# Optimization experiments

Hardware: AMD Instinct MI355X
Metric: run time of the kernel (lower is better)

Reference implementation:

```python
import jax, jax.numpy as jnp
import numpy as np


def setup_inputs() -> dict:
    key = jax.random.key(0)
    k1, k2 = jax.random.split(key)
    B, N, D = 4, 2048, 1024
    context = jax.random.normal(k1, (B, N, D), dtype=jnp.float32)
    # Dense(embedding_dim*3): kernel [D, 3D], bias [3D] (glorot-ish scale)
    W_qkv = jax.random.normal(k2, (D, 3 * D), dtype=jnp.float32) * (1.0 / np.sqrt(D))
    b_qkv = jnp.zeros((3 * D,), dtype=jnp.float32)
    return {"context": context, "W_qkv": W_qkv, "b_qkv": b_qkv}


def reference(context, W_qkv, b_qkv):
    B, N, D = context.shape
    qkv = context @ W_qkv + b_qkv                       # [B, N, 3D]
    q, k, v = jnp.split(qkv, 3, axis=-1)                # each [B, N, D]
    scores = jnp.einsum("bnd,bmd->bnm", q, k)           # [B, N, N]
    # Faithful quirk: original divides by sqrt(scores.shape[-1]) == sqrt(N)
    scores = scores / jnp.asarray(np.sqrt(N), dtype=scores.dtype)
    causal = jnp.tril(jnp.ones((N, N), dtype=jnp.float32))  # lower-triangular
    scores = jnp.where(causal == 0, -jnp.inf, scores)
    probs = jax.nn.softmax(scores, axis=-1)             # [B, N, N]
    out = jnp.einsum("bnm,bmd->bnd", probs, v)          # [B, N, D]
    return out
```

## Files before the change

kernel.cpp:

```cpp
#include <hip/hip_runtime.h>
#include <cstdint>
#include <cstddef>


typedef __attribute__((ext_vector_type(8))) __bf16 bf16x8;
typedef __attribute__((ext_vector_type(4))) float f32x4;

__device__ inline unsigned short f2bf(float f) {
  unsigned u = __float_as_uint(f);
  u = (u + 0x7FFFu + ((u >> 16) & 1u)) >> 16;
  return (unsigned short)u;
}

__device__ inline void gld16(const void* g, void* l) {
  __builtin_amdgcn_global_load_lds(
      (const __attribute__((address_space(1))) unsigned int*)g,
      (__attribute__((address_space(3))) unsigned int*)l, 16, 0, 0);
}

__device__ inline void stage_tiles(unsigned short* As, unsigned short* Bs,
                                   const unsigned short* Abase, long strideA,
                                   const unsigned short* Bbase, long strideB,
                                   int k0, int wave, int lrow, int lcol) {
#pragma unroll
  for (int c = 0; c < 4; c++) {
    const int q = wave * 4 + c;
    const int row = q * 8 + lrow;
    gld16(Abase + (size_t)row * strideA + k0 + lcol, &As[q * 512]);
    gld16(Bbase + (size_t)row * strideB + k0 + lcol, &Bs[q * 512]);
  }
}

__device__ inline void compute_tiles(const unsigned short* As, const unsigned short* Bs,
                                     int lane, int ry, int rx, f32x4 acc[4][4]) {
#pragma unroll
  for (int kk = 0; kk < 64; kk += 32) {
    const int cbase = (kk >> 3) + (lane >> 4);
    const int csw = ((cbase ^ (lane & 7)) << 3);
    bf16x8 a[4], b[4];
#pragma unroll
    for (int mi = 0; mi < 4; mi++)
      a[mi] = *(const bf16x8*)&As[(ry + mi * 16 + (lane & 15)) * 64 + csw];
#pragma unroll
    for (int nj = 0; nj < 4; nj++)
      b[nj] = *(const bf16x8*)&Bs[(rx + nj * 16 + (lane & 15)) * 64 + csw];
#pragma unroll
    for (int mi = 0; mi < 4; mi++)
#pragma unroll
      for (int nj = 0; nj < 4; nj++)
        acc[mi][nj] = __builtin_amdgcn_mfma_f32_16x16x32_bf16(b[nj], a[mi], acc[mi][nj], 0, 0, 0);
  }
}

__device__ inline void mma_mainloop(unsigned short* As, unsigned short* Bs,
                                    const unsigned short* Abase, long strideA,
                                    const unsigned short* Bbase, long strideB,
                                    int kIters, f32x4 acc[4][4]) {
  const int lane = threadIdx.x & 63, wave = threadIdx.x >> 6;
  const int ry = (wave >> 1) * 64, rx = (wave & 1) * 64;
  const int lrow = lane >> 3;
  const int lcol = ((lane & 7) ^ lrow) * 8;
#pragma unroll
  for (int mi = 0; mi < 4; mi++)
#pragma unroll
    for (int nj = 0; nj < 4; nj++) acc[mi][nj] = (f32x4)(0.f);
  for (int kt = 0; kt < kIters; kt++) {
    __syncthreads();
    stage_tiles(As, Bs, Abase, strideA, Bbase, strideB, kt * 64, wave, lrow, lcol);
    __syncthreads();
    compute_tiles(As, Bs, lane, ry, rx, acc);
  }
}

__device__ inline void mma_mainloop_db(unsigned short* As0, unsigned short* Bs0,
                                       unsigned short* As1, unsigned short* Bs1,
                                       const unsigned short* Abase, long strideA,
                                       const unsigned short* Bbase, long strideB,
                                       int kIters, f32x4 acc[4][4]) {
  const int lane = threadIdx.x & 63, wave = threadIdx.x >> 6;
  const int ry = (wave >> 1) * 64, rx = (wave & 1) * 64;
  const int lrow = lane >> 3;
  const int lcol = ((lane & 7) ^ lrow) * 8;
#pragma unroll
  for (int mi = 0; mi < 4; mi++)
#pragma unroll
    for (int nj = 0; nj < 4; nj++) acc[mi][nj] = (f32x4)(0.f);
  stage_tiles(As0, Bs0, Abase, strideA, Bbase, strideB, 0, wave, lrow, lcol);
  for (int kt = 0; kt < kIters; kt++) {
    __syncthreads();
    unsigned short* Asc = (kt & 1) ? As1 : As0;
    unsigned short* Bsc = (kt & 1) ? Bs1 : Bs0;
    if (kt + 1 < kIters) {
      unsigned short* Asn = (kt & 1) ? As0 : As1;
      unsigned short* Bsn = (kt & 1) ? Bs0 : Bs1;
      stage_tiles(Asn, Bsn, Abase, strideA, Bbase, strideB, (kt + 1) * 64, wave, lrow, lcol);
    }
    compute_tiles(Asc, Bsc, lane, ry, rx, acc);
  }
}


__global__ void k_convert(const float* __restrict__ x, unsigned short* __restrict__ y, int n4) {
  int i = blockIdx.x * blockDim.x + threadIdx.x;
  if (i >= n4) return;
  float4 v = ((const float4*)x)[i];
  ushort4 o;
  o.x = f2bf(v.x); o.y = f2bf(v.y); o.z = f2bf(v.z); o.w = f2bf(v.w);
  ((ushort4*)y)[i] = o;
}

__global__ void k_transpose_w(const float* __restrict__ W, unsigned short* __restrict__ Wt) {
  __shared__ unsigned short sm[64 * 65];
  const int n0 = blockIdx.x * 64;
  const int k0 = blockIdx.y * 64;
  for (int i = threadIdx.x; i < 4096; i += 256) {
    int r = i >> 6, c = i & 63;
    sm[c * 65 + r] = f2bf(W[(size_t)(k0 + r) * 3072 + n0 + c]);
  }
  __syncthreads();
  for (int i = threadIdx.x; i < 4096; i += 256) {
    int r = i >> 6, c = i & 63;
    Wt[(size_t)(n0 + r) * 1024 + k0 + c] = sm[r * 65 + c];
  }
}


__global__ __launch_bounds__(256) void k_gemm_qkv(const unsigned short* __restrict__ A,
                                                  const unsigned short* __restrict__ Wt,
                                                  const float* __restrict__ bias,
                                                  unsigned short* __restrict__ qk,
                                                  unsigned short* __restrict__ vT) {
  __shared__ unsigned short As[128 * 64];
  __shared__ unsigned short Bs[128 * 64];
  f32x4 acc[4][4];
  const int tM0 = blockIdx.y * 128;
  const int lane = threadIdx.x & 63, wave = threadIdx.x >> 6;
  const int ry = (wave >> 1) * 64, rx = (wave & 1) * 64;
  const int l16 = lane & 15, rq = lane >> 4;
  const bool isQK = blockIdx.x < 16;
  const int tN0 = isQK ? blockIdx.x * 128 : (blockIdx.x - 16) * 128;
  const unsigned short* Wtile = Wt + (size_t)(isQK ? tN0 : 2048 + tN0) * 1024;

  mma_mainloop(As, Bs, A + (size_t)tM0 * 1024, 1024, Wtile, 1024, 16, acc);

  if (isQK) {
#pragma unroll
    for (int mi = 0; mi < 4; mi++) {
      const int m = tM0 + ry + mi * 16 + l16;
#pragma unroll
      for (int nj = 0; nj < 4; nj++) {
        const int n = tN0 + rx + nj * 16 + rq * 4;
        const float4 bv = *(const float4*)&bias[n];
        ushort4 o;
        o.x = f2bf(acc[mi][nj][0] + bv.x);
        o.y = f2bf(acc[mi][nj][1] + bv.y);
        o.z = f2bf(acc[mi][nj][2] + bv.z);
        o.w = f2bf(acc[mi][nj][3] + bv.w);
        *(ushort4*)&qk[(size_t)m * 2048 + n] = o;
      }
    }
  } else {
#pragma unroll
    for (int mi = 0; mi < 4; mi++) {
      const int m = tM0 + ry + mi * 16 + l16;
      const int b = m >> 11, ns = m & 2047;
#pragma unroll
      for (int nj = 0; nj < 4; nj++) {
        const int d0 = tN0 + rx + nj * 16 + rq * 4;
        const float4 bv = *(const float4*)&bias[2048 + d0];
#pragma unroll
        for (int r = 0; r < 4; r++)
          vT[((size_t)(b * 1024 + d0 + r)) * 2048 + ns] = f2bf(acc[mi][nj][r] + ((const float*)&bv)[r]);
      }
    }
  }
}

__global__ __launch_bounds__(256) void k_scores(const unsigned short* __restrict__ qk,
                                                unsigned short* __restrict__ P,
                                                float* __restrict__ l, float scale) {
  __shared__ unsigned short As0[128 * 64], Bs0[128 * 64];
  __shared__ unsigned short As1[128 * 64], Bs1[128 * 64];
  const int t = blockIdx.x, b = blockIdx.z;
  int qb = (int)((sqrtf(8.0f * (float)t + 1.0f) - 1.0f) * 0.5f);
  while (qb * (qb + 1) / 2 > t) qb--;
  while ((qb + 1) * (qb + 2) / 2 <= t) qb++;
  const int kb = t - qb * (qb + 1) / 2;
  f32x4 acc[4][4];
  const unsigned short* Aq = qk + ((size_t)(b * 2048 + qb * 128)) * 2048;
  const unsigned short* Bk = qk + ((size_t)(b * 2048 + kb * 128)) * 2048 + 1024;
  mma_mainloop_db(As0, Bs0, As1, Bs1, Aq, 2048, Bk, 2048, 16, acc);
  const int lane = threadIdx.x & 63, wave = threadIdx.x >> 6;
  const int ry = (wave >> 1) * 64, rx = (wave & 1) * 64;
  const int l16 = lane & 15, rq = lane >> 4;
  unsigned short* Pb = P + ((size_t)(b * 2048 + qb * 128)) * 2048 + (size_t)kb * 128;
  float* lb = l + b * 2048 + qb * 128;
#pragma unroll
  for (int mi = 0; mi < 4; mi++) {
    const int m_local = ry + mi * 16 + l16;
    const int qi = qb * 128 + m_local;
    float rowpart = 0.f;
#pragma unroll
    for (int nj = 0; nj < 4; nj++) {
      const int n_base = rx + nj * 16 + rq * 4;
      ushort4 o;
      float p;
#pragma unroll
      for (int r = 0; r < 4; r++) {
        const int kj = kb * 128 + n_base + r;
        p = (kj <= qi) ? __expf(acc[mi][nj][r] * scale) : 0.f;
        rowpart += p;
        ((unsigned short*)&o)[r] = f2bf(p);
      }
      *(ushort4*)&Pb[(size_t)m_local * 2048 + n_base] = o;
    }
    rowpart += __shfl_xor(rowpart, 16, 64);
    rowpart += __shfl_xor(rowpart, 32, 64);
    if (rq == 0) atomicAdd(&lb[m_local], rowpart);
  }
}

__global__ __launch_bounds__(256) void k_pv(const unsigned short* __restrict__ P,
                                            const unsigned short* __restrict__ vT,
                                            const float* __restrict__ l,
                                            float* __restrict__ out) {
  __shared__ unsigned short As0[128 * 64], Bs0[128 * 64];
  __shared__ unsigned short As1[128 * 64], Bs1[128 * 64];
  const int db = blockIdx.x, b = blockIdx.z;
  int qb = blockIdx.y;
  if (b & 2) qb = 15 - qb;
  f32x4 acc[4][4];
  const unsigned short* Ap = P + ((size_t)(b * 2048 + qb * 128)) * 2048;
  const unsigned short* Bv = vT + ((size_t)(b * 1024 + db * 128)) * 2048;
  mma_mainloop_db(As0, Bs0, As1, Bs1, Ap, 2048, Bv, 2048, (qb + 1) * 2, acc);
  const int lane = threadIdx.x & 63, wave = threadIdx.x >> 6;
  const int ry = (wave >> 1) * 64, rx = (wave & 1) * 64;
  const int l16 = lane & 15, rq = lane >> 4;
  const float* lb = l + b * 2048 + qb * 128;
  float* ob = out + ((size_t)(b * 2048 + qb * 128)) * 1024 + db * 128;
#pragma unroll
  for (int mi = 0; mi < 4; mi++) {
    const int m_local = ry + mi * 16 + l16;
    const float inv = 1.0f / lb[m_local];
#pragma unroll
    for (int nj = 0; nj < 4; nj++) {
      const int n_base = rx + nj * 16 + rq * 4;
      float4 o;
      o.x = acc[mi][nj][0] * inv;
      o.y = acc[mi][nj][1] * inv;
      o.z = acc[mi][nj][2] * inv;
      o.w = acc[mi][nj][3] * inv;
      *(float4*)&ob[(size_t)m_local * 1024 + n_base] = o;
    }
  }
}


extern "C" void kernel_launch(void* const* d_in, const int* in_sizes, int n_in,
                              void* d_out, int out_size, void* d_ws, size_t ws_size,
                              hipStream_t stream) {
  const float* ctx  = (const float*)d_in[0];
  const float* W    = (const float*)d_in[1];
  const float* bias = (const float*)d_in[2];
  float* out = (float*)d_out;

  char* ws = (char*)d_ws;
  unsigned short* Actx = (unsigned short*)(ws + 0);
  unsigned short* Wt   = (unsigned short*)(ws + 16777216);
  unsigned short* qk   = (unsigned short*)(ws + 23068672);
  unsigned short* vT   = (unsigned short*)(ws + 56623104);
  unsigned short* P    = (unsigned short*)(ws + 73400320);
  float*          lsum = (float*)(ws + 106954752);

  hipMemsetAsync(lsum, 0, 4 * 2048 * sizeof(float), stream);
  k_convert<<<8192, 256, 0, stream>>>(ctx, Actx, (8192 * 1024) / 4);
  k_transpose_w<<<dim3(48, 16), 256, 0, stream>>>(W, Wt);
  k_gemm_qkv<<<dim3(24, 64), 256, 0, stream>>>(Actx, Wt, bias, qk, vT);
  k_scores<<<dim3(136, 1, 4), 256, 0, stream>>>(qk, P, lsum, 0.022097086912079608f);
  k_pv<<<dim3(8, 16, 4), 256, 0, stream>>>(P, vT, lsum, out);
}
```

Before: 284.4 us.

## Replace direct-to-LDS loads with register-relay prefetch pipeline and split QKV GEMM

The double-buffered mainloop used by the scores and PV kernels no longer uses global_load_lds. It now loads tiles two steps ahead into registers and writes them to LDS behind raw s_waitcnt/s_barrier pairs, so global latency overlaps more compute. The QKV projection is split into separate QK and V kernels, which removes the divergent epilogue branch but adds a launch. The change costs extra registers (16 uint4) and possible occupancy loss. Its LDS writes do not use the XOR swizzle layout that the global_load_lds path relied on, and that needs checking.

```diff
diff --git a/kernel.cpp b/kernel.cpp
--- a/kernel.cpp
+++ b/kernel.cpp
@@ -18,17 +18,8 @@
       (__attribute__((address_space(3))) unsigned int*)l, 16, 0, 0);
 }
 
-__device__ inline void stage_tiles(unsigned short* As, unsigned short* Bs,
-                                   const unsigned short* Abase, long strideA,
-                                   const unsigned short* Bbase, long strideB,
-                                   int k0, int wave, int lrow, int lcol) {
-#pragma unroll
-  for (int c = 0; c < 4; c++) {
-    const int q = wave * 4 + c;
-    const int row = q * 8 + lrow;
-    gld16(Abase + (size_t)row * strideA + k0 + lcol, &As[q * 512]);
-    gld16(Bbase + (size_t)row * strideB + k0 + lcol, &Bs[q * 512]);
-  }
+__device__ inline void raw_barrier_lds() {
+  asm volatile("s_waitcnt lgkmcnt(0)\n\ts_barrier" ::: "memory");
 }
 
 __device__ inline void compute_tiles(const unsigned short* As, const unsigned short* Bs,
@@ -65,18 +56,46 @@
 #pragma unroll
     for (int nj = 0; nj < 4; nj++) acc[mi][nj] = (f32x4)(0.f);
   for (int kt = 0; kt < kIters; kt++) {
+    const int k0 = kt * 64;
     __syncthreads();
-    stage_tiles(As, Bs, Abase, strideA, Bbase, strideB, kt * 64, wave, lrow, lcol);
+#pragma unroll
+    for (int c = 0; c < 4; c++) {
+      const int q = wave * 4 + c;
+      const int row = q * 8 + lrow;
+      gld16(Abase + (size_t)row * strideA + k0 + lcol, &As[q * 512]);
+      gld16(Bbase + (size_t)row * strideB + k0 + lcol, &Bs[q * 512]);
+    }
     __syncthreads();
     compute_tiles(As, Bs, lane, ry, rx, acc);
   }
 }
 
-__device__ inline void mma_mainloop_db(unsigned short* As0, unsigned short* Bs0,
-                                       unsigned short* As1, unsigned short* Bs1,
-                                       const unsigned short* Abase, long strideA,
-                                       const unsigned short* Bbase, long strideB,
-                                       int kIters, f32x4 acc[4][4]) {
+__device__ inline void relay_load(uint4 r[8],
+                                  const unsigned short* Abase, long sA,
+                                  const unsigned short* Bbase, long sB,
+                                  int k0, int wave, int lrow, int lcol) {
+#pragma unroll
+  for (int c = 0; c < 4; c++) {
+    const int row = (wave * 4 + c) * 8 + lrow;
+    r[c]     = *(const uint4*)(Abase + (size_t)row * sA + k0 + lcol);
+    r[4 + c] = *(const uint4*)(Bbase + (size_t)row * sB + k0 + lcol);
+  }
+}
+__device__ inline void relay_write(const uint4 r[8], unsigned short* As,
+                                   unsigned short* Bs, int wave, int lane) {
+#pragma unroll
+  for (int c = 0; c < 4; c++) {
+    const int q = wave * 4 + c;
+    *(uint4*)&As[q * 512 + lane * 8] = r[c];
+    *(uint4*)&Bs[q * 512 + lane * 8] = r[4 + c];
+  }
+}
+
+__device__ inline void mma_mainloop_relay(unsigned short* As0, unsigned short* Bs0,
+                                          unsigned short* As1, unsigned short* Bs1,
+                                          const unsigned short* Abase, long sA,
+                                          const unsigned short* Bbase, long sB,
+                                          int kIters, f32x4 acc[4][4]) {
   const int lane = threadIdx.x & 63, wave = threadIdx.x >> 6;
   const int ry = (wave >> 1) * 64, rx = (wave & 1) * 64;
   const int lrow = lane >> 3;
@@ -85,15 +104,25 @@
   for (int mi = 0; mi < 4; mi++)
 #pragma unroll
     for (int nj = 0; nj < 4; nj++) acc[mi][nj] = (f32x4)(0.f);
-  stage_tiles(As0, Bs0, Abase, strideA, Bbase, strideB, 0, wave, lrow, lcol);
+
+  uint4 ra[8], rb[8];
+  relay_load(ra, Abase, sA, Bbase, sB, 0, wave, lrow, lcol);
+  if (kIters > 1) relay_load(rb, Abase, sA, Bbase, sB, 64, wave, lrow, lcol);
+  relay_write(ra, As0, Bs0, wave, lane);
+  raw_barrier_lds();
+
   for (int kt = 0; kt < kIters; kt++) {
-    __syncthreads();
-    unsigned short* Asc = (kt & 1) ? As1 : As0;
-    unsigned short* Bsc = (kt & 1) ? Bs1 : Bs0;
+    const bool odd = kt & 1;
+    unsigned short* Asc = odd ? As1 : As0;
+    unsigned short* Bsc = odd ? Bs1 : Bs0;
     if (kt + 1 < kIters) {
-      unsigned short* Asn = (kt & 1) ? As0 : As1;
-      unsigned short* Bsn = (kt & 1) ? Bs0 : Bs1;
-      stage_tiles(Asn, Bsn, Abase, strideA, Bbase, strideB, (kt + 1) * 64, wave, lrow, lcol);
+      unsigned short* Asn = odd ? As0 : As1;
+      unsigned short* Bsn = odd ? Bs0 : Bs1;
+      raw_barrier_lds();
+      relay_write(odd ? ra : rb, Asn, Bsn, wave, lane);
+      if (kt + 2 < kIters)
+        relay_load(odd ? rb : ra, Abase, sA, Bbase, sB, (kt + 2) * 64, wave, lrow, lcol);
+      raw_barrier_lds();
     }
     compute_tiles(Asc, Bsc, lane, ry, rx, acc);
   }
@@ -125,53 +154,64 @@
 }
 
 
-__global__ __launch_bounds__(256) void k_gemm_qkv(const unsigned short* __restrict__ A,
-                                                  const unsigned short* __restrict__ Wt,
-                                                  const float* __restrict__ bias,
-                                                  unsigned short* __restrict__ qk,
-                                                  unsigned short* __restrict__ vT) {
+__global__ __launch_bounds__(256) void k_gemm_qk(const unsigned short* __restrict__ A,
+                                                 const unsigned short* __restrict__ Wt,
+                                                 const float* __restrict__ bias,
+                                                 unsigned short* __restrict__ qk) {
   __shared__ unsigned short As[128 * 64];
   __shared__ unsigned short Bs[128 * 64];
   f32x4 acc[4][4];
+  const int tN0 = blockIdx.x * 128;
   const int tM0 = blockIdx.y * 128;
+  mma_mainloop(As, Bs, A + (size_t)tM0 * 1024, 1024, Wt + (size_t)tN0 * 1024, 1024, 16, acc);
   const int lane = threadIdx.x & 63, wave = threadIdx.x >> 6;
   const int ry = (wave >> 1) * 64, rx = (wave & 1) * 64;
   const int l16 = lane & 15, rq = lane >> 4;
-  const bool isQK = blockIdx.x < 16;
-  const int tN0 = isQK ? blockIdx.x * 128 : (blockIdx.x - 16) * 128;
-  const unsigned short* Wtile = Wt + (size_t)(isQK ? tN0 : 2048 + tN0) * 1024;
-
-  mma_mainloop(As, Bs, A + (size_t)tM0 * 1024, 1024, Wtile, 1024, 16, acc);
-
-  if (isQK) {
-#pragma unroll
-    for (int mi = 0; mi < 4; mi++) {
-      const int m = tM0 + ry + mi * 16 + l16;
-#pragma unroll
-      for (int nj = 0; nj < 4; nj++) {
-        const int n = tN0 + rx + nj * 16 + rq * 4;
-        const float4 bv = *(const float4*)&bias[n];
-        ushort4 o;
-        o.x = f2bf(acc[mi][nj][0] + bv.x);
-        o.y = f2bf(acc[mi][nj][1] + bv.y);
-        o.z = f2bf(acc[mi][nj][2] + bv.z);
-        o.w = f2bf(acc[mi][nj][3] + bv.w);
-        *(ushort4*)&qk[(size_t)m * 2048 + n] = o;
-      }
-    }
-  } else {
-#pragma unroll
-    for (int mi = 0; mi < 4; mi++) {
-      const int m = tM0 + ry + mi * 16 + l16;
-      const int b = m >> 11, ns = m & 2047;
-#pragma unroll
-      for (int nj = 0; nj < 4; nj++) {
-        const int d0 = tN0 + rx + nj * 16 + rq * 4;
-        const float4 bv = *(const float4*)&bias[2048 + d0];
-#pragma unroll
-        for (int r = 0; r < 4; r++)
-          vT[((size_t)(b * 1024 + d0 + r)) * 2048 + ns] = f2bf(acc[mi][nj][r] + ((const float*)&bv)[r]);
-      }
+#pragma unroll
+  for (int mi = 0; mi < 4; mi++) {
+    const int m = tM0 + ry + mi * 16 + l16;
+#pragma unroll
+    for (int nj = 0; nj < 4; nj++) {
+      const int n = tN0 + rx + nj * 16 + rq * 4;
+      const float4 bv = *(const float4*)&bias[n];
+      ushort4 o;
+      o.x = f2bf(acc[mi][nj][0] + bv.x);
+      o.y = f2bf(acc[mi][nj][1] + bv.y);
+      o.z = f2bf(acc[mi][nj][2] + bv.z);
+      o.w = f2bf(acc[mi][nj][3] + bv.w);
+      *(ushort4*)&qk[(size_t)m * 2048 + n] = o;
+    }
+  }
+}
+
+__global__ __launch_bounds__(256) void k_gemm_v(const unsigned short* __restrict__ A,
+                                                const unsigned short* __restrict__ Wt,
+                                                const float* __restrict__ bias,
+                                                unsigned short* __restrict__ vT) {
+  __shared__ unsigned short As[128 * 64];
+  __shared__ unsigned short Bs[128 * 64];
+  f32x4 acc[4][4];
+  const int tN0 = blockIdx.x * 128;
+  const int tM0 = blockIdx.y * 128;
+  mma_mainloop(As, Bs, A + (size_t)tM0 * 1024, 1024,
+               Wt + (size_t)(2048 + tN0) * 1024, 1024, 16, acc);
+  int tM0v = tM0;
+  asm volatile("" : "+v"(tM0v));
+  const int lane = threadIdx.x & 63, wave = threadIdx.x >> 6;
+  const int ry = (wave >> 1) * 64, rx = (wave & 1) * 64;
+  const int l16 = lane & 15, rq = lane >> 4;
+#pragma unroll
+  for (int mi = 0; mi < 4; mi++) {
+    const int m = tM0v + ry + mi * 16 + l16;
+    const int b = m >> 11, ns = m & 2047;
+#pragma unroll
+    for (int nj = 0; nj < 4; nj++) {
+      const int d0 = tN0 + rx + nj * 16 + rq * 4;
+      const float4 bv = *(const float4*)&bias[2048 + d0];
+#pragma unroll
+      for (int r = 0; r < 4; r++)
+        vT[((size_t)(b * 1024 + d0 + r)) * 2048 + ns] =
+            f2bf(acc[mi][nj][r] + ((const float*)&bv)[r]);
     }
   }
 }
@@ -189,7 +229,7 @@
   f32x4 acc[4][4];
   const unsigned short* Aq = qk + ((size_t)(b * 2048 + qb * 128)) * 2048;
   const unsigned short* Bk = qk + ((size_t)(b * 2048 + kb * 128)) * 2048 + 1024;
-  mma_mainloop_db(As0, Bs0, As1, Bs1, Aq, 2048, Bk, 2048, 16, acc);
+  mma_mainloop_relay(As0, Bs0, As1, Bs1, Aq, 2048, Bk, 2048, 16, acc);
   const int lane = threadIdx.x & 63, wave = threadIdx.x >> 6;
   const int ry = (wave >> 1) * 64, rx = (wave & 1) * 64;
   const int l16 = lane & 15, rq = lane >> 4;
@@ -232,7 +272,7 @@
   f32x4 acc[4][4];
   const unsigned short* Ap = P + ((size_t)(b * 2048 + qb * 128)) * 2048;
   const unsigned short* Bv = vT + ((size_t)(b * 1024 + db * 128)) * 2048;
-  mma_mainloop_db(As0, Bs0, As1, Bs1, Ap, 2048, Bv, 2048, (qb + 1) * 2, acc);
+  mma_mainloop_relay(As0, Bs0, As1, Bs1, Ap, 2048, Bv, 2048, (qb + 1) * 2, acc);
   const int lane = threadIdx.x & 63, wave = threadIdx.x >> 6;
   const int ry = (wave >> 1) * 64, rx = (wave & 1) * 64;
   const int l16 = lane & 15, rq = lane >> 4;
@@ -275,7 +315,8 @@
   hipMemsetAsync(lsum, 0, 4 * 2048 * sizeof(float), stream);
   k_convert<<<8192, 256, 0, stream>>>(ctx, Actx, (8192 * 1024) / 4);
   k_transpose_w<<<dim3(48, 16), 256, 0, stream>>>(W, Wt);
-  k_gemm_qkv<<<dim3(24, 64), 256, 0, stream>>>(Actx, Wt, bias, qk, vT);
+  k_gemm_qk<<<dim3(16, 64), 256, 0, stream>>>(Actx, Wt, bias, qk);
+  k_gemm_v<<<dim3(8, 64), 256, 0, stream>>>(Actx, Wt, bias, vT);
   k_scores<<<dim3(136, 1, 4), 256, 0, stream>>>(qk, P, lsum, 0.022097086912079608f);
   k_pv<<<dim3(8, 16, 4), 256, 0, stream>>>(P, vT, lsum, out);
 }
```

New measurement: 400.4 us. +40.8%, slower.
